# Kernel optimization log

Hardware: AMD Instinct MI355X
Metric: run time of the kernel (lower is better)

Reference implementation:

```python
import jax, jax.numpy as jnp
import numpy as np

N = 100000      # num nodes
E = 3200000     # num edges (avg degree 32)
D = 64          # feature dim
K = 3           # propagation steps (self._k)
ALPHA = 0.1     # convex combine (self._alpha)
EPS = 1e-6      # PNY norm epsilon


def setup_inputs() -> dict:
    key = jax.random.key(0)
    k1, k2, k3 = jax.random.split(key, 3)
    feat = jax.random.normal(k1, (N, D), dtype=jnp.float32)
    src = jax.random.randint(k2, (E,), 0, N)
    dst = jax.random.randint(k3, (E,), 0, N)
    return {"feat": feat, "src": src, "dst": dst}


def reference(feat, src, dst):
    n = feat.shape[0]
    e = src.shape[0]
    ones = jnp.ones((e,), dtype=feat.dtype)
    out_deg = jax.ops.segment_sum(ones, src, num_segments=n)  # [N]
    in_deg = jax.ops.segment_sum(ones, dst, num_segments=n)   # [N]
    src_norm = jnp.power(jnp.clip(out_deg, 1.0, None), -0.5)[:, None]  # [N,1]
    dst_norm = jnp.power(jnp.clip(in_deg, 1.0, None), -0.5)[:, None]   # [N,1]

    feat_0 = feat
    for _ in range(K):
        feat = feat * src_norm                 # degree-norm scale on source side
        prev_x = feat                          # prev_x = clone(feat)
        # u_mul_e('h','w','m') with w==1 + fn.sum: edge-weighted sparse aggregation
        agg = jax.ops.segment_sum(feat[src], dst, num_segments=n)  # [N,D]
        # PNY_Norm(prev_x, agg): per-node L2-norm-preserving rescale of aggregate
        pn = jnp.linalg.norm(prev_x, axis=-1, keepdims=True)
        an = jnp.linalg.norm(agg, axis=-1, keepdims=True)
        feat = agg * (pn / (an + EPS))
        feat = feat * dst_norm                 # degree-norm scale on dest side
        feat = (1.0 - ALPHA) * feat + ALPHA * feat_0  # convex combine with feat_0
    return feat
```

## Files before the change

kernel.cpp:

```cpp
#include <hip/hip_runtime.h>
#include <hip/hip_fp16.h>
#include <math.h>

#define ALPHA 0.1f
#define EPS 1e-6f
#define D 64
#define CH 8192
#define BUCK_SH 8

__global__ void hist_kernel(const int* __restrict__ src, const int* __restrict__ dst,
                            int* __restrict__ hist_d, int* __restrict__ hist_s,
                            int nbuck, int nblk, int E) {
    __shared__ int hd[512], hs[512];
    int t = threadIdx.x, b = blockIdx.x;
    for (int u = t; u < 512; u += 256) { hd[u] = 0; hs[u] = 0; }
    __syncthreads();
    int beg = b * CH, end = min(beg + CH, E);
    for (int e = beg + t; e < end; e += 256) {
        atomicAdd(&hd[dst[e] >> BUCK_SH], 1);
        atomicAdd(&hs[src[e] >> BUCK_SH], 1);
    }
    __syncthreads();
    for (int u = t; u < nbuck; u += 256) {
        hist_d[u * nblk + b] = hd[u];
        hist_s[u * nblk + b] = hs[u];
    }
}

__global__ void bucket_total_kernel(const int* __restrict__ hist_d, const int* __restrict__ hist_s,
                                    int* __restrict__ tot_d, int* __restrict__ tot_s, int nblk) {
    __shared__ int rd[256], rs[256];
    int u = blockIdx.x, t = threadIdx.x;
    int sd = 0, ss = 0;
    for (int b = t; b < nblk; b += 256) {
        sd += hist_d[u * nblk + b];
        ss += hist_s[u * nblk + b];
    }
    rd[t] = sd; rs[t] = ss;
    __syncthreads();
    for (int off = 128; off; off >>= 1) {
        if (t < off) { rd[t] += rd[t + off]; rs[t] += rs[t + off]; }
        __syncthreads();
    }
    if (t == 0) { tot_d[u] = rd[0]; tot_s[u] = rs[0]; }
}

__global__ void base_scan_kernel(const int* __restrict__ tot_d, const int* __restrict__ tot_s,
                                 int* __restrict__ base_d, int* __restrict__ base_s, int nbuck) {
    __shared__ int a[512], b[512];
    int t = threadIdx.x;
    int vd = (t < nbuck) ? tot_d[t] : 0;
    int vs = (t < nbuck) ? tot_s[t] : 0;
    a[t] = vd; b[t] = vs;
    __syncthreads();
    for (int off = 1; off < 512; off <<= 1) {
        int av = (t >= off) ? a[t - off] : 0;
        int bv = (t >= off) ? b[t - off] : 0;
        __syncthreads();
        a[t] += av; b[t] += bv;
        __syncthreads();
    }
    if (t < nbuck) {
        base_d[t] = a[t] - vd;
        base_s[t] = b[t] - vs;
    }
}

__global__ void row_scan_kernel(const int* __restrict__ hist_d, const int* __restrict__ hist_s,
                                const int* __restrict__ base_d, const int* __restrict__ base_s,
                                int* __restrict__ sbase_d, int* __restrict__ sbase_s,
                                int nblk, int E, int m) {
    __shared__ int a[512], b[512];
    int u = blockIdx.x, t = threadIdx.x;
    int hd = (t < nblk) ? hist_d[u * nblk + t] : 0;
    int hs = (t < nblk) ? hist_s[u * nblk + t] : 0;
    a[t] = hd; b[t] = hs;
    __syncthreads();
    for (int off = 1; off < 512; off <<= 1) {
        int av = (t >= off) ? a[t - off] : 0;
        int bv = (t >= off) ? b[t - off] : 0;
        __syncthreads();
        a[t] += av; b[t] += bv;
        __syncthreads();
    }
    if (t < nblk) {
        sbase_d[u * nblk + t] = base_d[u] + a[t] - hd;
        sbase_s[u * nblk + t] = base_s[u] + b[t] - hs;
    }
    if (u == 0 && t == 0) { sbase_d[m] = E; sbase_s[m] = E; }
}

__global__ void scatter_kernel(const int* __restrict__ src, const int* __restrict__ dst,
                               const int* __restrict__ sbase_d, const int* __restrict__ sbase_s,
                               unsigned* __restrict__ pairs, unsigned char* __restrict__ skeys,
                               int nbuck, int nblk, int E) {
    __shared__ int cd[512], cs[512];
    int t = threadIdx.x, b = blockIdx.x;
    for (int u = t; u < nbuck; u += 256) {
        cd[u] = sbase_d[u * nblk + b];
        cs[u] = sbase_s[u * nblk + b];
    }
    __syncthreads();
    int beg = b * CH, end = min(beg + CH, E);
    for (int e = beg + t; e < end; e += 256) {
        int dv = dst[e], sv = src[e];
        int pu = atomicAdd(&cd[dv >> BUCK_SH], 1);
        pairs[pu] = ((unsigned)(dv & 255) << 24) | (unsigned)sv;
        int su = atomicAdd(&cs[sv >> BUCK_SH], 1);
        skeys[su] = (unsigned char)(sv & 255);
    }
}

__global__ void src_deg_kernel(const unsigned char* __restrict__ skeys,
                               const int* __restrict__ sbase_s,
                               float* __restrict__ sn, int nbuck, int nblk, int n) {
    __shared__ int lh[256];
    int t = threadIdx.x, u = blockIdx.x;
    lh[t] = 0;
    __syncthreads();
    int beg = sbase_s[u * nblk];
    int end = sbase_s[(u + 1) * nblk];
    for (int i = beg + t; i < end; i += 256) atomicAdd(&lh[skeys[i]], 1);
    __syncthreads();
    int node = (u << BUCK_SH) + t;
    if (node < n) sn[node] = rsqrtf(fmaxf((float)lh[t], 1.0f));
}

__global__ void build_kernel(const unsigned* __restrict__ pairs, const int* __restrict__ sbase_d,
                             int* __restrict__ rowptr, int* __restrict__ csr,
                             float* __restrict__ dn, int nbuck, int nblk, int n, int E) {
    __shared__ int lh[256], le[256], cnt[256];
    int t = threadIdx.x, u = blockIdx.x;
    lh[t] = 0; cnt[t] = 0;
    __syncthreads();
    int beg = sbase_d[u * nblk];
    int end = sbase_d[(u + 1) * nblk];
    for (int i = beg + t; i < end; i += 256) atomicAdd(&lh[pairs[i] >> 24], 1);
    __syncthreads();
    int c0 = lh[t];
    for (int off = 1; off < 256; off <<= 1) {
        int x = (t >= off) ? lh[t - off] : 0;
        __syncthreads();
        lh[t] += x;
        __syncthreads();
    }
    le[t] = lh[t] - c0;
    __syncthreads();
    int node = (u << BUCK_SH) + t;
    if (node < n) {
        rowptr[node] = beg + le[t];
        dn[node] = rsqrtf(fmaxf((float)c0, 1.0f));
    }
    if (u == nbuck - 1 && t == 0) rowptr[n] = E;
    for (int i = beg + t; i < end; i += 256) {
        unsigned pr = pairs[i];
        int bb = pr >> 24;
        int p = atomicAdd(&cnt[bb], 1);
        csr[beg + le[bb] + p] = (int)(pr & 0xFFFFFFu);
    }
}

__global__ void prescale_kernel(const float* __restrict__ feat, const float* __restrict__ sn,
                                __half* __restrict__ outh, float* __restrict__ pn, int n) {
    int row  = blockIdx.x * (blockDim.x >> 6) + (threadIdx.x >> 6);
    int lane = threadIdx.x & 63;
    if (row >= n) return;
    float x = feat[(long)row * D + lane];
    float ss = x * x;
    #pragma unroll
    for (int off = 32; off; off >>= 1) ss += __shfl_xor(ss, off, 64);
    float s = sn[row];
    float v = x * s;
    float vp = __shfl_xor(v, 1, 64);
    if (!(lane & 1)) {
        *(__half2*)(outh + (long)row * D + lane) = __floats2half2_rn(v, vp);
    }
    if (lane == 0) pn[row] = s * sqrtf(ss);
}

template <int LAST>
__global__ void iter_kernel(const __half* __restrict__ cur, const float* __restrict__ feat0,
                            const int* __restrict__ rowptr, const int* __restrict__ csr_src,
                            const float* __restrict__ pn, const float* __restrict__ dn,
                            const float* __restrict__ sn,
                            __half* __restrict__ nexth, float* __restrict__ npn,
                            float* __restrict__ out, int n) {
    int row  = blockIdx.x * (blockDim.x >> 6) + (threadIdx.x >> 6);
    int lane = threadIdx.x & 63;
    if (row >= n) return;
    int g = lane >> 3, sub = lane & 7;

    float acc[8] = {0.f, 0.f, 0.f, 0.f, 0.f, 0.f, 0.f, 0.f};
    int beg = rowptr[row], end = rowptr[row + 1];
    for (int base = beg; base < end; base += 64) {
        int m = end - base; if (m > 64) m = 64;
        int s_l = (lane < m) ? csr_src[base + lane] : 0;
        int nj = (m + 7) >> 3;
        #pragma unroll 4
        for (int j = 0; j < nj; ++j) {
            int e = j * 8 + g;
            int s = __shfl(s_l, e, 64);
            if (e < m) {
                int4 raw = *(const int4*)(cur + (long)s * D + sub * 8);
                float2 f0 = __half22float2(*(__half2*)&raw.x);
                float2 f1 = __half22float2(*(__half2*)&raw.y);
                float2 f2 = __half22float2(*(__half2*)&raw.z);
                float2 f3 = __half22float2(*(__half2*)&raw.w);
                acc[0] += f0.x; acc[1] += f0.y;
                acc[2] += f1.x; acc[3] += f1.y;
                acc[4] += f2.x; acc[5] += f2.y;
                acc[6] += f3.x; acc[7] += f3.y;
            }
        }
    }
    #pragma unroll
    for (int i = 0; i < 8; ++i) {
        float a = acc[i];
        a += __shfl_xor(a, 8, 64);
        a += __shfl_xor(a, 16, 64);
        a += __shfl_xor(a, 32, 64);
        acc[i] = a;
    }
    float dd = 0.f;
    #pragma unroll
    for (int i = 0; i < 8; ++i) dd += acc[i] * acc[i];
    dd += __shfl_xor(dd, 1, 64);
    dd += __shfl_xor(dd, 2, 64);
    dd += __shfl_xor(dd, 4, 64);
    float an = sqrtf(dd);
    float scale = pn[row] / (an + EPS) * dn[row] * (1.0f - ALPHA);

    if (g == 0) {
        long fb = (long)row * D + sub * 8;
        float4 f0a = *(const float4*)(feat0 + fb);
        float4 f0b = *(const float4*)(feat0 + fb + 4);
        float nx[8];
        nx[0] = acc[0] * scale + ALPHA * f0a.x;
        nx[1] = acc[1] * scale + ALPHA * f0a.y;
        nx[2] = acc[2] * scale + ALPHA * f0a.z;
        nx[3] = acc[3] * scale + ALPHA * f0a.w;
        nx[4] = acc[4] * scale + ALPHA * f0b.x;
        nx[5] = acc[5] * scale + ALPHA * f0b.y;
        nx[6] = acc[6] * scale + ALPHA * f0b.z;
        nx[7] = acc[7] * scale + ALPHA * f0b.w;
        if (LAST) {
            float4 o0 = {nx[0], nx[1], nx[2], nx[3]};
            float4 o1 = {nx[4], nx[5], nx[6], nx[7]};
            *(float4*)(out + fb) = o0;
            *(float4*)(out + fb + 4) = o1;
        } else {
            float s = sn[row];
            __half2 h0 = __floats2half2_rn(nx[0] * s, nx[1] * s);
            __half2 h1 = __floats2half2_rn(nx[2] * s, nx[3] * s);
            __half2 h2 = __floats2half2_rn(nx[4] * s, nx[5] * s);
            __half2 h3 = __floats2half2_rn(nx[6] * s, nx[7] * s);
            int4 packed;
            packed.x = *(int*)&h0; packed.y = *(int*)&h1;
            packed.z = *(int*)&h2; packed.w = *(int*)&h3;
            *(int4*)(nexth + fb) = packed;
            float nn = 0.f;
            #pragma unroll
            for (int i = 0; i < 8; ++i) nn += nx[i] * nx[i];
            nn += __shfl_xor(nn, 1, 64);
            nn += __shfl_xor(nn, 2, 64);
            nn += __shfl_xor(nn, 4, 64);
            if (sub == 0) npn[row] = s * sqrtf(nn);
        }
    }
}

extern "C" void kernel_launch(void* const* d_in, const int* in_sizes, int n_in,
                              void* d_out, int out_size, void* d_ws, size_t ws_size,
                              hipStream_t stream) {
    const float* feat = (const float*)d_in[0];
    const int*   src  = (const int*)d_in[1];
    const int*   dst  = (const int*)d_in[2];
    float* out = (float*)d_out;

    int n = in_sizes[0] / D;
    int E = in_sizes[1];

    int nbuck = (n + 255) >> BUCK_SH;
    int nblk  = (E + CH - 1) / CH;
    int m     = nbuck * nblk;

    int* hist_d  = (int*)d_ws;
    int* hist_s  = hist_d + m;
    int* sbase_d = hist_s + m;
    int* sbase_s = sbase_d + m + 1;
    int* tot_d   = sbase_s + m + 1;
    int* tot_s   = tot_d + 512;
    int* base_d  = tot_s + 512;
    int* base_s  = base_d + 512;
    int* rowptr  = base_s + 512;
    float* sn    = (float*)(rowptr + n + 1);
    float* dn    = sn + n;
    float* pn_a  = dn + n;
    float* pn_b  = pn_a + n;

    size_t used4 = (size_t)(4 * m + 2) + 2048 + 5 * (size_t)n + 1;
    size_t offP  = (used4 * 4 + 255) & ~(size_t)255;
    unsigned* pairs  = (unsigned*)((char*)d_ws + offP);
    __half* scaled_a = (__half*)((char*)d_ws + offP);
    __half* scaled_b = scaled_a + (size_t)n * D;
    size_t szP = 2 * (size_t)n * D * sizeof(__half);
    size_t offQ = (offP + szP + 255) & ~(size_t)255;
    unsigned char* skeys = (unsigned char*)d_ws + offQ;
    int* csr = (int*)((char*)d_ws + offQ);

    int eblocks = nblk;
    hist_kernel<<<eblocks, 256, 0, stream>>>(src, dst, hist_d, hist_s, nbuck, nblk, E);
    bucket_total_kernel<<<nbuck, 256, 0, stream>>>(hist_d, hist_s, tot_d, tot_s, nblk);
    base_scan_kernel<<<1, 512, 0, stream>>>(tot_d, tot_s, base_d, base_s, nbuck);
    row_scan_kernel<<<nbuck, 512, 0, stream>>>(hist_d, hist_s, base_d, base_s,
                                               sbase_d, sbase_s, nblk, E, m);
    scatter_kernel<<<eblocks, 256, 0, stream>>>(src, dst, sbase_d, sbase_s, pairs, skeys,
                                                nbuck, nblk, E);
    src_deg_kernel<<<nbuck, 256, 0, stream>>>(skeys, sbase_s, sn, nbuck, nblk, n);
    build_kernel<<<nbuck, 256, 0, stream>>>(pairs, sbase_d, rowptr, csr, dn, nbuck, nblk, n, E);

    int blocks = (n + 3) / 4;
    prescale_kernel<<<blocks, 256, 0, stream>>>(feat, sn, scaled_a, pn_a, n);
    iter_kernel<0><<<blocks, 256, 0, stream>>>(scaled_a, feat, rowptr, csr, pn_a, dn, sn,
                                               scaled_b, pn_b, nullptr, n);
    iter_kernel<0><<<blocks, 256, 0, stream>>>(scaled_b, feat, rowptr, csr, pn_b, dn, sn,
                                               scaled_a, pn_a, nullptr, n);
    iter_kernel<1><<<blocks, 256, 0, stream>>>(scaled_a, feat, rowptr, csr, pn_a, dn, sn,
                                               nullptr, nullptr, out, n);
}
```

Before: 336.5 us.

## Map one row per 8-lane group in SpMM and accumulate in half2

The aggregation kernel now gives each 8-lane group its own destination row, so a wave handles 8 rows instead of one. This removes the cross-group shuffle reduction and the idle lanes in the epilogue. Accumulation switches from fp32 to packed half2 adds, which cuts instruction count but risks precision loss and overflow over about 32 neighbours. The source-degree kernel is also merged into the build kernel to save a launch. Groups within a wave can now diverge, since the loop runs to the largest degree among the wave's 8 rows.

```diff
diff --git a/kernel.cpp b/kernel.cpp
--- a/kernel.cpp
+++ b/kernel.cpp
@@ -111,28 +111,18 @@
     }
 }
 
-__global__ void src_deg_kernel(const unsigned char* __restrict__ skeys,
-                               const int* __restrict__ sbase_s,
-                               float* __restrict__ sn, int nbuck, int nblk, int n) {
-    __shared__ int lh[256];
+__global__ void build_kernel(const unsigned* __restrict__ pairs, const int* __restrict__ sbase_d,
+                             const unsigned char* __restrict__ skeys, const int* __restrict__ sbase_s,
+                             int* __restrict__ rowptr, int* __restrict__ csr,
+                             float* __restrict__ dn, float* __restrict__ sn,
+                             int nbuck, int nblk, int n, int E) {
+    __shared__ int lh[256], le[256], cnt[256], lhs[256];
     int t = threadIdx.x, u = blockIdx.x;
-    lh[t] = 0;
-    __syncthreads();
-    int beg = sbase_s[u * nblk];
-    int end = sbase_s[(u + 1) * nblk];
-    for (int i = beg + t; i < end; i += 256) atomicAdd(&lh[skeys[i]], 1);
-    __syncthreads();
-    int node = (u << BUCK_SH) + t;
-    if (node < n) sn[node] = rsqrtf(fmaxf((float)lh[t], 1.0f));
-}
-
-__global__ void build_kernel(const unsigned* __restrict__ pairs, const int* __restrict__ sbase_d,
-                             int* __restrict__ rowptr, int* __restrict__ csr,
-                             float* __restrict__ dn, int nbuck, int nblk, int n, int E) {
-    __shared__ int lh[256], le[256], cnt[256];
-    int t = threadIdx.x, u = blockIdx.x;
-    lh[t] = 0; cnt[t] = 0;
-    __syncthreads();
+    lh[t] = 0; cnt[t] = 0; lhs[t] = 0;
+    __syncthreads();
+    int sb = sbase_s[u * nblk];
+    int se = sbase_s[(u + 1) * nblk];
+    for (int i = sb + t; i < se; i += 256) atomicAdd(&lhs[skeys[i]], 1);
     int beg = sbase_d[u * nblk];
     int end = sbase_d[(u + 1) * nblk];
     for (int i = beg + t; i < end; i += 256) atomicAdd(&lh[pairs[i] >> 24], 1);
@@ -150,6 +140,7 @@
     if (node < n) {
         rowptr[node] = beg + le[t];
         dn[node] = rsqrtf(fmaxf((float)c0, 1.0f));
+        sn[node] = rsqrtf(fmaxf((float)lhs[t], 1.0f));
     }
     if (u == nbuck - 1 && t == 0) rowptr[n] = E;
     for (int i = beg + t; i < end; i += 256) {
@@ -185,87 +176,83 @@
                             const float* __restrict__ sn,
                             __half* __restrict__ nexth, float* __restrict__ npn,
                             float* __restrict__ out, int n) {
-    int row  = blockIdx.x * (blockDim.x >> 6) + (threadIdx.x >> 6);
+    int wid  = blockIdx.x * (blockDim.x >> 6) + (threadIdx.x >> 6);
     int lane = threadIdx.x & 63;
-    if (row >= n) return;
     int g = lane >> 3, sub = lane & 7;
-
-    float acc[8] = {0.f, 0.f, 0.f, 0.f, 0.f, 0.f, 0.f, 0.f};
-    int beg = rowptr[row], end = rowptr[row + 1];
-    for (int base = beg; base < end; base += 64) {
-        int m = end - base; if (m > 64) m = 64;
-        int s_l = (lane < m) ? csr_src[base + lane] : 0;
-        int nj = (m + 7) >> 3;
-        #pragma unroll 4
-        for (int j = 0; j < nj; ++j) {
-            int e = j * 8 + g;
-            int s = __shfl(s_l, e, 64);
-            if (e < m) {
-                int4 raw = *(const int4*)(cur + (long)s * D + sub * 8);
-                float2 f0 = __half22float2(*(__half2*)&raw.x);
-                float2 f1 = __half22float2(*(__half2*)&raw.y);
-                float2 f2 = __half22float2(*(__half2*)&raw.z);
-                float2 f3 = __half22float2(*(__half2*)&raw.w);
-                acc[0] += f0.x; acc[1] += f0.y;
-                acc[2] += f1.x; acc[3] += f1.y;
-                acc[4] += f2.x; acc[5] += f2.y;
-                acc[6] += f3.x; acc[7] += f3.y;
+    int row = wid * 8 + g;
+    bool valid = row < n;
+    int beg = valid ? rowptr[row] : 0;
+    int end = valid ? rowptr[row + 1] : 0;
+    int deg = end - beg;
+    int dmax = deg;
+    dmax = max(dmax, __shfl_xor(dmax, 8, 64));
+    dmax = max(dmax, __shfl_xor(dmax, 16, 64));
+    dmax = max(dmax, __shfl_xor(dmax, 32, 64));
+
+    unsigned subOff = (unsigned)sub * 16u;
+    __half2 hz = __float2half2_rn(0.f);
+    __half2 hacc0 = hz, hacc1 = hz, hacc2 = hz, hacc3 = hz;
+    for (int j0 = 0; j0 < dmax; j0 += 4) {
+        #pragma unroll
+        for (int k = 0; k < 4; ++k) {
+            int j = j0 + k;
+            if (j < deg) {
+                int s = csr_src[beg + j];
+                int4 raw = *(const int4*)((const char*)cur + (unsigned)s * 128u + subOff);
+                hacc0 = __hadd2(hacc0, *(const __half2*)&raw.x);
+                hacc1 = __hadd2(hacc1, *(const __half2*)&raw.y);
+                hacc2 = __hadd2(hacc2, *(const __half2*)&raw.z);
+                hacc3 = __hadd2(hacc3, *(const __half2*)&raw.w);
             }
         }
     }
-    #pragma unroll
-    for (int i = 0; i < 8; ++i) {
-        float a = acc[i];
-        a += __shfl_xor(a, 8, 64);
-        a += __shfl_xor(a, 16, 64);
-        a += __shfl_xor(a, 32, 64);
-        acc[i] = a;
-    }
-    float dd = 0.f;
-    #pragma unroll
-    for (int i = 0; i < 8; ++i) dd += acc[i] * acc[i];
-    dd += __shfl_xor(dd, 1, 64);
-    dd += __shfl_xor(dd, 2, 64);
-    dd += __shfl_xor(dd, 4, 64);
-    float an = sqrtf(dd);
+    if (!valid) return;
+
+    float2 f0 = __half22float2(hacc0);
+    float2 f1 = __half22float2(hacc1);
+    float2 f2 = __half22float2(hacc2);
+    float2 f3 = __half22float2(hacc3);
+    float a0 = f0.x, a1 = f0.y, a2 = f1.x, a3 = f1.y;
+    float a4 = f2.x, a5 = f2.y, a6 = f3.x, a7 = f3.y;
+    float ss = a0*a0 + a1*a1 + a2*a2 + a3*a3 + a4*a4 + a5*a5 + a6*a6 + a7*a7;
+    ss += __shfl_xor(ss, 1, 64);
+    ss += __shfl_xor(ss, 2, 64);
+    ss += __shfl_xor(ss, 4, 64);
+    float an = sqrtf(ss);
     float scale = pn[row] / (an + EPS) * dn[row] * (1.0f - ALPHA);
 
-    if (g == 0) {
-        long fb = (long)row * D + sub * 8;
-        float4 f0a = *(const float4*)(feat0 + fb);
-        float4 f0b = *(const float4*)(feat0 + fb + 4);
-        float nx[8];
-        nx[0] = acc[0] * scale + ALPHA * f0a.x;
-        nx[1] = acc[1] * scale + ALPHA * f0a.y;
-        nx[2] = acc[2] * scale + ALPHA * f0a.z;
-        nx[3] = acc[3] * scale + ALPHA * f0a.w;
-        nx[4] = acc[4] * scale + ALPHA * f0b.x;
-        nx[5] = acc[5] * scale + ALPHA * f0b.y;
-        nx[6] = acc[6] * scale + ALPHA * f0b.z;
-        nx[7] = acc[7] * scale + ALPHA * f0b.w;
-        if (LAST) {
-            float4 o0 = {nx[0], nx[1], nx[2], nx[3]};
-            float4 o1 = {nx[4], nx[5], nx[6], nx[7]};
-            *(float4*)(out + fb) = o0;
-            *(float4*)(out + fb + 4) = o1;
-        } else {
-            float s = sn[row];
-            __half2 h0 = __floats2half2_rn(nx[0] * s, nx[1] * s);
-            __half2 h1 = __floats2half2_rn(nx[2] * s, nx[3] * s);
-            __half2 h2 = __floats2half2_rn(nx[4] * s, nx[5] * s);
-            __half2 h3 = __floats2half2_rn(nx[6] * s, nx[7] * s);
-            int4 packed;
-            packed.x = *(int*)&h0; packed.y = *(int*)&h1;
-            packed.z = *(int*)&h2; packed.w = *(int*)&h3;
-            *(int4*)(nexth + fb) = packed;
-            float nn = 0.f;
-            #pragma unroll
-            for (int i = 0; i < 8; ++i) nn += nx[i] * nx[i];
-            nn += __shfl_xor(nn, 1, 64);
-            nn += __shfl_xor(nn, 2, 64);
-            nn += __shfl_xor(nn, 4, 64);
-            if (sub == 0) npn[row] = s * sqrtf(nn);
-        }
+    long fb = (long)row * D + sub * 8;
+    float4 f0a = *(const float4*)(feat0 + fb);
+    float4 f0b = *(const float4*)(feat0 + fb + 4);
+    float nx0 = a0 * scale + ALPHA * f0a.x;
+    float nx1 = a1 * scale + ALPHA * f0a.y;
+    float nx2 = a2 * scale + ALPHA * f0a.z;
+    float nx3 = a3 * scale + ALPHA * f0a.w;
+    float nx4 = a4 * scale + ALPHA * f0b.x;
+    float nx5 = a5 * scale + ALPHA * f0b.y;
+    float nx6 = a6 * scale + ALPHA * f0b.z;
+    float nx7 = a7 * scale + ALPHA * f0b.w;
+    if (LAST) {
+        float4 o0 = {nx0, nx1, nx2, nx3};
+        float4 o1 = {nx4, nx5, nx6, nx7};
+        *(float4*)(out + fb) = o0;
+        *(float4*)(out + fb + 4) = o1;
+    } else {
+        float s = sn[row];
+        __half2 h0 = __floats2half2_rn(nx0 * s, nx1 * s);
+        __half2 h1 = __floats2half2_rn(nx2 * s, nx3 * s);
+        __half2 h2 = __floats2half2_rn(nx4 * s, nx5 * s);
+        __half2 h3 = __floats2half2_rn(nx6 * s, nx7 * s);
+        int4 packed;
+        packed.x = *(int*)&h0; packed.y = *(int*)&h1;
+        packed.z = *(int*)&h2; packed.w = *(int*)&h3;
+        *(int4*)(nexth + fb) = packed;
+        float nn = nx0*nx0 + nx1*nx1 + nx2*nx2 + nx3*nx3
+                 + nx4*nx4 + nx5*nx5 + nx6*nx6 + nx7*nx7;
+        nn += __shfl_xor(nn, 1, 64);
+        nn += __shfl_xor(nn, 2, 64);
+        nn += __shfl_xor(nn, 4, 64);
+        if (sub == 0) npn[row] = s * sqrtf(nn);
     }
 }
 
@@ -316,15 +303,16 @@
                                                sbase_d, sbase_s, nblk, E, m);
     scatter_kernel<<<eblocks, 256, 0, stream>>>(src, dst, sbase_d, sbase_s, pairs, skeys,
                                                 nbuck, nblk, E);
-    src_deg_kernel<<<nbuck, 256, 0, stream>>>(skeys, sbase_s, sn, nbuck, nblk, n);
-    build_kernel<<<nbuck, 256, 0, stream>>>(pairs, sbase_d, rowptr, csr, dn, nbuck, nblk, n, E);
-
-    int blocks = (n + 3) / 4;
-    prescale_kernel<<<blocks, 256, 0, stream>>>(feat, sn, scaled_a, pn_a, n);
-    iter_kernel<0><<<blocks, 256, 0, stream>>>(scaled_a, feat, rowptr, csr, pn_a, dn, sn,
-                                               scaled_b, pn_b, nullptr, n);
-    iter_kernel<0><<<blocks, 256, 0, stream>>>(scaled_b, feat, rowptr, csr, pn_b, dn, sn,
-                                               scaled_a, pn_a, nullptr, n);
-    iter_kernel<1><<<blocks, 256, 0, stream>>>(scaled_a, feat, rowptr, csr, pn_a, dn, sn,
-                                               nullptr, nullptr, out, n);
-}
+    build_kernel<<<nbuck, 256, 0, stream>>>(pairs, sbase_d, skeys, sbase_s,
+                                            rowptr, csr, dn, sn, nbuck, nblk, n, E);
+
+    int pblocks = (n + 3) / 4;
+    prescale_kernel<<<pblocks, 256, 0, stream>>>(feat, sn, scaled_a, pn_a, n);
+    int iblocks = (n + 31) / 32;
+    iter_kernel<0><<<iblocks, 256, 0, stream>>>(scaled_a, feat, rowptr, csr, pn_a, dn, sn,
+                                                scaled_b, pn_b, nullptr, n);
+    iter_kernel<0><<<iblocks, 256, 0, stream>>>(scaled_b, feat, rowptr, csr, pn_b, dn, sn,
+                                                scaled_a, pn_a, nullptr, n);
+    iter_kernel<1><<<iblocks, 256, 0, stream>>>(scaled_a, feat, rowptr, csr, pn_a, dn, sn,
+                                                nullptr, nullptr, out, n);
+}
```

After: 354.5 us. 5.3% more time.
